# Kernel tuning notes

Measured on AMD Instinct MI355X. Metric: run time of the kernel, lower is better.

The kernel has to match this reference:

```python
import jax, jax.numpy as jnp
import numpy as np

G, R, M, H, NH, OUT = 2048, 1024, 1024, 256, 8, 2
DH = H // NH


def _ln(x, g, b):
    m = jnp.mean(x, -1, keepdims=True)
    v = jnp.var(x, -1, keepdims=True)
    return (x - m) * jax.lax.rsqrt(v + 1e-5) * g + b


def _mha(xq, xkv, w, mask=None):
    # w: [4, H, H] = (Wq, Wk, Wv, Wo); mask: [Nq, Nk] bool (True = attend)
    q = (xq @ w[0]).reshape(-1, NH, DH)
    k = (xkv @ w[1]).reshape(-1, NH, DH)
    v = (xkv @ w[2]).reshape(-1, NH, DH)
    s = jnp.einsum('qhd,khd->hqk', q, k) * np.float32(1.0 / np.sqrt(DH))
    if mask is not None:
        s = jnp.where(mask[None], s, jnp.float32(-1e9))
    a = jax.nn.softmax(s, -1)
    ctx = jnp.einsum('hqk,khd->qhd', a, v).reshape(xq.shape[0], H)
    return ctx @ w[3]


def setup_inputs() -> dict:
    key = jax.random.key(0)
    ks = jax.random.split(key, 32)
    sc = np.float32(1.0 / np.sqrt(H))

    def n(i, shape, s=sc):
        return jax.random.normal(ks[i], shape, jnp.float32) * s

    inp = {}
    inp['gene_emb'] = n(0, (G, H), 0.02)
    inp['reaction_emb'] = n(1, (R, H), 0.02)
    inp['metab_emb'] = n(2, (M, H), 0.02)
    # PreProcessor (note: torch code reuses ONE LayerNorm instance -> shared params)
    inp['pre_w1'] = n(3, (H, H)); inp['pre_b1'] = jnp.zeros((H,), jnp.float32)
    inp['pre_w2'] = n(4, (H, H)); inp['pre_b2'] = jnp.zeros((H,), jnp.float32)
    inp['pre_ln_g'] = jnp.ones((H,), jnp.float32); inp['pre_ln_b'] = jnp.zeros((H,), jnp.float32)
    # NSA: 'M' block = masked attention per edge type (4), 'S' block = full self-attn per node type (3)
    inp['wm'] = n(5, (4, 4, H, H))
    inp['ws'] = n(6, (3, 4, H, H))
    inp['ln_g'] = jnp.ones((3, H), jnp.float32); inp['ln_b'] = jnp.zeros((3, H), jnp.float32)
    # AttentionalGraphAggregation
    inp['gate_w1'] = n(7, (H, H // 2)); inp['gate_b1'] = jnp.zeros((H // 2,), jnp.float32)
    inp['gate_w2'] = n(8, (H // 2, 1)); inp['gate_b2'] = jnp.zeros((1,), jnp.float32)
    inp['tr_w'] = n(9, (H, H)); inp['tr_b'] = jnp.zeros((H,), jnp.float32)
    # prediction head: num_layers=1 -> single Linear
    inp['head_w'] = n(10, (H, OUT)); inp['head_b'] = jnp.zeros((OUT,), jnp.float32)
    # dense edge masks (sparse biological graphs)
    inp['adj_pp'] = jax.random.bernoulli(ks[11], 0.01, (G, G))
    inp['adj_rr'] = jax.random.bernoulli(ks[12], 0.01, (G, G))
    inp['inc_gpr'] = jax.random.bernoulli(ks[13], 0.01, (R, G))
    inp['adj_mm'] = jax.random.bernoulli(ks[14], 0.01, (M, M))
    return inp


def reference(gene_emb, reaction_emb, metab_emb, pre_w1, pre_b1, pre_w2, pre_b2,
              pre_ln_g, pre_ln_b, wm, ws, ln_g, ln_b, gate_w1, gate_b1, gate_w2,
              gate_b2, tr_w, tr_b, head_w, head_b, adj_pp, adj_rr, inc_gpr, adj_mm):
    # preprocessor MLP on gene embeddings (single-graph path; dropout=eval/identity)
    h = jax.nn.relu(_ln(gene_emb @ pre_w1 + pre_b1, pre_ln_g, pre_ln_b))
    xg = jax.nn.relu(_ln(h @ pre_w2 + pre_b2, pre_ln_g, pre_ln_b))
    xr, xm = reaction_emb, metab_emb
    # 'M' block: masked cross/self attention per edge type, sum-aggregated per dst type
    mg = _mha(xg, xg, wm[0], adj_pp) + _mha(xg, xg, wm[1], adj_rr)
    mr = _mha(xr, xg, wm[2], inc_gpr)
    mm = _mha(xm, xm, wm[3], adj_mm)
    xg, xr, xm = xg + mg, xr + mr, xm + mm
    # 'S' block: full self-attention within each node set
    xg = xg + _mha(xg, xg, ws[0])
    xr = xr + _mha(xr, xr, ws[1])
    xm = xm + _mha(xm, xm, ws[2])
    # per-node-type layer norms (gene branch feeds the head)
    xg = _ln(xg, ln_g[0], ln_b[0])
    # attentional graph aggregation over gene nodes (single graph -> plain softmax)
    gate = jax.nn.relu(xg @ gate_w1 + gate_b1) @ gate_w2 + gate_b2  # [G, 1]
    a = jax.nn.softmax(gate, 0)
    t = jax.nn.relu(xg @ tr_w + tr_b)
    pooled = jnp.sum(a * t, 0, keepdims=True)  # [1, H]
    return pooled @ head_w + head_b  # [1, OUT]
```

## Files before the change

kernel.cpp:

```cpp
#include <hip/hip_runtime.h>
#include <hip/hip_bf16.h>
#include <cmath>
#include <cstdint>

typedef unsigned int u32;
typedef unsigned char u8;
typedef unsigned short ushort;
typedef __attribute__((ext_vector_type(8))) short short8;
typedef __attribute__((ext_vector_type(4))) float f32x4;
typedef __attribute__((ext_vector_type(16))) float f32x16;
typedef __attribute__((ext_vector_type(4))) unsigned short us4;

#define Gn 2048
#define Hd 256
#define CSTRIDE 192

static __device__ __forceinline__ ushort f2bf(float x) {
    __hip_bfloat16 b = __float2bfloat16(x);
    return *reinterpret_cast<ushort*>(&b);
}
static __device__ __forceinline__ float bf2f(ushort u) {
    return __uint_as_float(((u32)u) << 16);
}


template <int BETA, int OUTMODE, int QKVMODE, int KT, int LNF, int LNRELU, int WRA>
static __device__ __forceinline__ void gemm_body(
    const int bx, const int by, const int bz,
    const float* __restrict__ A, int lda,
    const ushort* __restrict__ bt_hi, const ushort* __restrict__ bt_lo,
    int slot0, int slot2, const float* __restrict__ bias,
    const float* __restrict__ lng, const float* __restrict__ lnb,
    float* __restrict__ C, int N, float* __restrict__ Aout)
{
    const int tid = threadIdx.x;
    const int wv = tid >> 6, l = tid & 63;
    const int lr = l & 15, lg = l >> 4;
    const int row = bx * 32 + wv * 16 + lr;
    const int col0 = by * 64;
    int slot = slot0, zq = 0, buf = 0;
    if (QKVMODE == 1) { slot = slot0 + bz + bz / 3; zq = bz % 3; buf = bz / 3; }
    else if (QKVMODE == 2) { slot = slot0 + bz; zq = bz; }
    const ushort* bhb = bt_hi + (long)slot * 65536;
    const ushort* blb = bt_lo + (long)slot * 65536;
    const float* arow = A + (long)row * lda;

    float mean = 0.f, rs = 0.f;
    if (LNF) {
        float s = 0.f, s2 = 0.f;
        #pragma unroll
        for (int ks = 0; ks < 8; ++ks) {
            const float4 a0 = *(const float4*)&arow[ks * 32 + lg * 8];
            const float4 a1 = *(const float4*)&arow[ks * 32 + lg * 8 + 4];
            s  += (a0.x + a0.y) + (a0.z + a0.w) + (a1.x + a1.y) + (a1.z + a1.w);
            s2 += a0.x * a0.x + a0.y * a0.y + a0.z * a0.z + a0.w * a0.w +
                  a1.x * a1.x + a1.y * a1.y + a1.z * a1.z + a1.w * a1.w;
        }
        s += __shfl_xor(s, 16);  s += __shfl_xor(s, 32);
        s2 += __shfl_xor(s2, 16); s2 += __shfl_xor(s2, 32);
        mean = s * (1.f / 256.f);
        rs = rsqrtf(s2 * (1.f / 256.f) - mean * mean + 1e-5f);
    }

    const f32x4 z4 = {0.f, 0.f, 0.f, 0.f};
    f32x4 acc[4] = {z4, z4, z4, z4};

    #pragma unroll
    for (int ks = 0; ks < KT / 32; ++ks) {
        const int k0 = ks * 32;
        const ushort* bh; const ushort* bl; int kbi = ks;
        if (KT == 512 && k0 >= 256) {
            bh = bt_hi + (long)slot2 * 65536;
            bl = bt_lo + (long)slot2 * 65536;
            kbi = ks - 8;
        } else { bh = bhb; bl = blb; }
        float av[8];
        *(float4*)&av[0] = *(const float4*)&arow[k0 + lg * 8];
        *(float4*)&av[4] = *(const float4*)&arow[k0 + lg * 8 + 4];
        if (LNF) {
            float gvv[8], bvv[8];
            *(float4*)&gvv[0] = *(const float4*)&lng[k0 + lg * 8];
            *(float4*)&gvv[4] = *(const float4*)&lng[k0 + lg * 8 + 4];
            *(float4*)&bvv[0] = *(const float4*)&lnb[k0 + lg * 8];
            *(float4*)&bvv[4] = *(const float4*)&lnb[k0 + lg * 8 + 4];
            #pragma unroll
            for (int j = 0; j < 8; ++j) {
                float v = (av[j] - mean) * rs * gvv[j] + bvv[j];
                if (LNRELU) v = fmaxf(v, 0.f);
                av[j] = v;
            }
            if (WRA && by == 0 && bz == 0) {
                *(float4*)&Aout[(long)row * 256 + k0 + lg * 8] = *(float4*)&av[0];
                *(float4*)&Aout[(long)row * 256 + k0 + lg * 8 + 4] = *(float4*)&av[4];
            }
        }
        short8 ahi, alo;
        #pragma unroll
        for (int j = 0; j < 8; ++j) {
            const u32 bi = __float_as_uint(av[j]);
            ahi[j] = (short)(bi >> 16);
            const float fh = __uint_as_float(bi & 0xffff0000u);
            alo[j] = (short)f2bf(av[j] - fh);
        }
        #pragma unroll
        for (int f = 0; f < 4; ++f) {
            const long bo = (long)(((by * 4 + f) * 8 + kbi) << 9) + (l << 3);
            const short8 bhi = *(const short8*)&bh[bo];
            const short8 blo = *(const short8*)&bl[bo];
            acc[f] = __builtin_amdgcn_mfma_f32_16x16x32_bf16(ahi, bhi, acc[f], 0, 0, 0);
            acc[f] = __builtin_amdgcn_mfma_f32_16x16x32_bf16(alo, bhi, acc[f], 0, 0, 0);
            acc[f] = __builtin_amdgcn_mfma_f32_16x16x32_bf16(ahi, blo, acc[f], 0, 0, 0);
        }
    }

    const float QS = 0.17677669529663687f * 1.4426950408889634f;

    #pragma unroll
    for (int f = 0; f < 4; ++f) {
        const int col = col0 + f * 16 + lr;
        const float bv = bias ? bias[col] : 0.f;
        #pragma unroll
        for (int r = 0; r < 4; ++r) {
            const int rr = bx * 32 + wv * 16 + lg * 4 + r;
            float v = acc[f][r] + bv;
            if (OUTMODE == 1) {
                if (zq == 0) v *= QS;
                ushort* ob = (ushort*)C + (long)buf * 1572864;
                const int h = col >> 5, d = col & 31;
                if (QKVMODE == 1 || zq < 2)
                    ob[zq * 524288 + ((h * 2048 + rr) << 5) + d] = f2bf(v);
                else
                    ob[1048576 + ((h * 32 + d) << 11) + rr] = f2bf(v);
            } else {
                if (BETA) v += C[(long)rr * N + col];
                C[(long)rr * N + col] = v;
            }
        }
    }
}

__global__ __launch_bounds__(256) void mergedA_kernel(
    const u8* __restrict__ adj, int* __restrict__ det0, int* __restrict__ det1,
    const float* __restrict__ pre_w1, const float* __restrict__ pre_w2,
    const float* __restrict__ wm, const float* __restrict__ wsw,
    const float* __restrict__ gate_w1, const float* __restrict__ tr_w,
    ushort* __restrict__ bt_hi, ushort* __restrict__ bt_lo,
    u32* __restrict__ ticket)
{
    __shared__ float T[32][257];
    __shared__ int sd0[4], sd1[4];
    const int tid = threadIdx.x;
    if (blockIdx.x == 0 && tid == 0) *ticket = 0;
    if (blockIdx.x < 64) {
        const int idx = blockIdx.x * 256 + tid;
        const uint4 w = ((const uint4*)adj)[idx];
        int c0 = ((w.x & 0xffu) ? 1 : 0) + ((w.y & 0xffu) ? 1 : 0) +
                 ((w.z & 0xffu) ? 1 : 0) + ((w.w & 0xffu) ? 1 : 0);
        int c1 = ((w.x & 0xffffff00u) ? 1 : 0) + ((w.y & 0xffffff00u) ? 1 : 0) +
                 ((w.z & 0xffffff00u) ? 1 : 0) + ((w.w & 0xffffff00u) ? 1 : 0);
        #pragma unroll
        for (int o = 1; o < 64; o <<= 1) { c0 += __shfl_xor(c0, o); c1 += __shfl_xor(c1, o); }
        if ((tid & 63) == 0) { sd0[tid >> 6] = c0; sd1[tid >> 6] = c1; }
        __syncthreads();
        if (tid == 0) {
            det0[blockIdx.x] = sd0[0] + sd0[1] + sd0[2] + sd0[3];
            det1[blockIdx.x] = sd1[0] + sd1[1] + sd1[2] + sd1[3];
        }
        return;
    }
    const int b2 = blockIdx.x - 64;
    const int slot = b2 >> 3;
    const int kb = b2 & 7;
    const int k0 = kb * 32;
    const float* src; int ncols = 256;
    if (slot == 0) src = pre_w1;
    else if (slot == 1) src = pre_w2;
    else if (slot < 6) src = wm + (long)(slot - 2) * 65536;
    else if (slot < 10) src = wm + (long)(4 + slot - 6) * 65536;
    else if (slot < 14) src = wsw + (long)(slot - 10) * 65536;
    else if (slot == 14) { src = gate_w1; ncols = 128; }
    else src = tr_w;

    const int lsh = (ncols == 256) ? 6 : 5;
    const int tot = 32 << lsh;
    for (int i = tid; i < tot; i += 256) {
        const int kk = i >> lsh, c4 = (i & ((1 << lsh) - 1)) << 2;
        const float4 v = *(const float4*)&src[(long)(k0 + kk) * ncols + c4];
        T[kk][c4 + 0] = v.x; T[kk][c4 + 1] = v.y;
        T[kk][c4 + 2] = v.z; T[kk][c4 + 3] = v.w;
    }
    __syncthreads();
    if (tid < ncols) {
        ushort hb[32], lb[32];
        #pragma unroll
        for (int kk = 0; kk < 32; ++kk) {
            const float x = T[kk][tid];
            const u32 bi = __float_as_uint(x);
            const ushort h = (ushort)(bi >> 16);
            const float fh = __uint_as_float(bi & 0xffff0000u);
            hb[kk] = h; lb[kk] = f2bf(x - fh);
        }
        const int cb = tid >> 4, lr = tid & 15;
        const long base = (long)slot * 65536 + ((cb * 8 + kb) << 9);
        ushort* oh = bt_hi + base;
        ushort* ol = bt_lo + base;
        #pragma unroll
        for (int lg2 = 0; lg2 < 4; ++lg2) {
            const int off = (lg2 * 16 + lr) << 3;
            *(uint4*)&oh[off] = *(const uint4*)&hb[lg2 * 8];
            *(uint4*)&ol[off] = *(const uint4*)&lb[lg2 * 8];
        }
    }
}

__global__ __launch_bounds__(128) void mergedB_kernel(
    const u8* __restrict__ src0, const u8* __restrict__ src1,
    const int* __restrict__ det0, const int* __restrict__ det1,
    u32* __restrict__ bits, int* __restrict__ deg, int* __restrict__ colidx,
    const float* __restrict__ gene_emb,
    const ushort* __restrict__ bt_hi, const ushort* __restrict__ bt_lo,
    const float* __restrict__ pre_b1, float* __restrict__ tmp0)
{
    __shared__ u32 sw[128];
    const int tid = threadIdx.x;
    if (blockIdx.x < 2048) {
        const int lane = tid & 63;
        int c0 = det0[lane], c1 = det1[lane];
        #pragma unroll
        for (int o = 1; o < 64; o <<= 1) { c0 += __shfl_xor(c0, o); c1 += __shfl_xor(c1, o); }
        const int f = (c0 > 0) ? ((c1 > 0) ? 1 : 0) : 2;
        const int W = blockIdx.x * 128 + tid;
        const int z = W >> 17;
        const int rem = W & 131071;
        const int row = rem >> 6, w = rem & 63;
// ... 25 lines not shown
            const uint4* p = (const uint4*)((const float*)src + (long)row * 2048 + w * 32);
            #pragma unroll
            for (int j = 0; j < 8; ++j) {
                const uint4 q = p[j];
                v |= ((q.x & 0x7fffffffu) ? 1u : 0u) << (j * 4 + 0);
                v |= ((q.y & 0x7fffffffu) ? 1u : 0u) << (j * 4 + 1);
                v |= ((q.z & 0x7fffffffu) ? 1u : 0u) << (j * 4 + 2);
                v |= ((q.w & 0x7fffffffu) ? 1u : 0u) << (j * 4 + 3);
            }
        }
        bits[(long)z * 131072 + rem] = v;
        sw[tid] = v;
        __syncthreads();
        if (tid < 2) {
            const int rem0 = (blockIdx.x * 128) & 131071;
            const int r = (rem0 >> 6) + tid;
            int* ci = colidx + ((long)z * 2048 + r) * CSTRIDE;
            int d = 0;
            #pragma unroll 4
            for (int ww = 0; ww < 64; ++ww) {
                u32 x = sw[tid * 64 + ww];
                while (x) {
                    const int j = __ffs(x) - 1;
                    if (d < CSTRIDE) ci[d] = ww * 32 + j;
                    ++d;
                    x &= x - 1;
                }
            }
            deg[z * 2048 + r] = d < CSTRIDE ? d : CSTRIDE;
        }
        return;
    }
    const int b2 = blockIdx.x - 2048;
    gemm_body<0, 0, 0, 256, 0, 0, 0>(b2 >> 2, b2 & 3, 0, gene_emb, 256,
                                     bt_hi, bt_lo, 0, 0, pre_b1,
                                     nullptr, nullptr, tmp0, 256, nullptr);
}

__global__ __launch_bounds__(128) void mergedC_kernel(
    const float* __restrict__ tmp0,
    const ushort* __restrict__ bt_hi, const ushort* __restrict__ bt_lo,
    const float* __restrict__ pre_b2, const float* __restrict__ pre_ln_g,
    const float* __restrict__ pre_ln_b, float* __restrict__ tmp1)
{
    const int b2 = blockIdx.x;
    gemm_body<0, 0, 0, 256, 1, 1, 0>(b2 >> 2, b2 & 3, 0, tmp0, 256,
                                     bt_hi, bt_lo, 1, 0, pre_b2,
                                     pre_ln_g, pre_ln_b, tmp1, 256, nullptr);
}

__global__ __launch_bounds__(128) void qkvm_kernel(
    const float* __restrict__ tmp1,
    const ushort* __restrict__ bt_hi, const ushort* __restrict__ bt_lo,
    const float* __restrict__ pre_ln_g, const float* __restrict__ pre_ln_b,
    float* __restrict__ qkvb, float* __restrict__ xg1)
{
    gemm_body<0, 1, 1, 256, 1, 1, 1>(blockIdx.x, blockIdx.y, blockIdx.z,
                                     tmp1, 256, bt_hi, bt_lo, 2, 0, nullptr,
                                     pre_ln_g, pre_ln_b, qkvb, 256, xg1);
}
__global__ __launch_bounds__(128) void wo_m_kernel(
    const float* __restrict__ ctx2,
    const ushort* __restrict__ bt_hi, const ushort* __restrict__ bt_lo,
    float* __restrict__ xg1)
{
    gemm_body<1, 0, 0, 512, 0, 0, 0>(blockIdx.x, blockIdx.y, 0, ctx2, 512,
                                     bt_hi, bt_lo, 5, 9, nullptr,
                                     nullptr, nullptr, xg1, 256, nullptr);
}
__global__ __launch_bounds__(128) void qkvs_kernel(
    const float* __restrict__ xg1,
    const ushort* __restrict__ bt_hi, const ushort* __restrict__ bt_lo,
    float* __restrict__ qkvb)
{
    gemm_body<0, 1, 2, 256, 0, 0, 0>(blockIdx.x, blockIdx.y, blockIdx.z,
                                     xg1, 256, bt_hi, bt_lo, 10, 0, nullptr,
                                     nullptr, nullptr, qkvb, 256, nullptr);
}
__global__ __launch_bounds__(128) void wo_s_kernel(
    const float* __restrict__ ctx2,
    const ushort* __restrict__ bt_hi, const ushort* __restrict__ bt_lo,
    float* __restrict__ xg1)
{
    gemm_body<1, 0, 0, 256, 0, 0, 0>(blockIdx.x, blockIdx.y, 0, ctx2, 512,
                                     bt_hi, bt_lo, 13, 0, nullptr,
                                     nullptr, nullptr, xg1, 256, nullptr);
}

__global__ __launch_bounds__(64) void attn_sparse_kernel(
    const ushort* __restrict__ qkvb, const int* __restrict__ deg,
    const int* __restrict__ colidx, float* __restrict__ ctx)
{
    const int r = blockIdx.x, z = blockIdx.y;
    const ushort* qb = qkvb + (long)z * 1572864;
    const ushort* kb = qb + 524288;
    const ushort* vr = qb + 1048576;
    const int l = threadIdx.x;
    const int h = l >> 3, dg = l & 7;
    float* orow = &ctx[(long)r * 512 + z * 256 + h * 32 + dg * 4];
    const int n = deg[z * 2048 + r];
    if (n == 0) {
        float a0 = 0.f, a1 = 0.f, a2 = 0.f, a3 = 0.f;
        for (int k = 0; k < 2048; ++k) {
            const us4 vv = *(const us4*)&vr[((h * 2048 + k) << 5) + dg * 4];
            a0 += bf2f(vv[0]); a1 += bf2f(vv[1]); a2 += bf2f(vv[2]); a3 += bf2f(vv[3]);
        }
        float4 o; const float inv = 1.f / 2048.f;
        o.x = a0 * inv; o.y = a1 * inv; o.z = a2 * inv; o.w = a3 * inv;
        *(float4*)orow = o;
        return;
    }
    float q0, q1, q2, q3;
    {
        const us4 qv = *(const us4*)&qb[((h * 2048 + r) << 5) + dg * 4];
        q0 = bf2f(qv[0]); q1 = bf2f(qv[1]); q2 = bf2f(qv[2]); q3 = bf2f(qv[3]);
    }
    const int* ci = colidx + ((long)z * 2048 + r) * CSTRIDE;
    float m = -INFINITY, lsum = 0.f;
    float a0 = 0.f, a1 = 0.f, a2 = 0.f, a3 = 0.f;
    int kn = ci[0];
    us4 kv = *(const us4*)&kb[((h * 2048 + kn) << 5) + dg * 4];
    us4 vv = *(const us4*)&vr[((h * 2048 + kn) << 5) + dg * 4];
    for (int e = 0; e < n; ++e) {
        const us4 kc = kv, vc = vv;
        if (e + 1 < n) {
            kn = ci[e + 1];
            kv = *(const us4*)&kb[((h * 2048 + kn) << 5) + dg * 4];
            vv = *(const us4*)&vr[((h * 2048 + kn) << 5) + dg * 4];
        }
        float s = q0 * bf2f(kc[0]) + q1 * bf2f(kc[1]) +
                  q2 * bf2f(kc[2]) + q3 * bf2f(kc[3]);
        s += __shfl_xor(s, 1); s += __shfl_xor(s, 2); s += __shfl_xor(s, 4);
        const float mn = fmaxf(m, s);
        const float fac = __builtin_amdgcn_exp2f(m - mn);
        const float p = __builtin_amdgcn_exp2f(s - mn);
        lsum = lsum * fac + p;
        a0 = a0 * fac + p * bf2f(vc[0]);
        a1 = a1 * fac + p * bf2f(vc[1]);
        a2 = a2 * fac + p * bf2f(vc[2]);
        a3 = a3 * fac + p * bf2f(vc[3]);
        m = mn;
    }
    const float inv = 1.f / lsum;
    float4 o; o.x = a0 * inv; o.y = a1 * inv; o.z = a2 * inv; o.w = a3 * inv;
    *(float4*)orow = o;
}

__global__ __launch_bounds__(512) void attn_dense_kernel(
    const ushort* __restrict__ qkvb, float* __restrict__ ctx)
{
    const ushort* qb = qkvb;
    const ushort* kb = qb + 524288;
    const ushort* vt = qb + 1048576;
    const int h = blockIdx.x, qt = blockIdx.y;
    const int wv = threadIdx.x >> 6;
    const int l = threadIdx.x & 63;
    const int lq = l & 31;
    const int hi = l >> 5;
    const int qglob = qt * 32 + lq;

    __shared__ float Mm[8][32], Ml[8][32];
    __shared__ float Macc[8][64][17];
    __shared__ float ctile[32][33];

    const int qoff = ((h * 2048 + qglob) << 5) + hi * 8;
    const short8 qf0 = *(const short8*)&qb[qoff];
    const short8 qf1 = *(const short8*)&qb[qoff + 16];

    float m = -INFINITY, lsum = 0.f;
    f32x16 acc, zz16;
    #pragma unroll
    for (int i = 0; i < 16; ++i) { acc[i] = 0.f; zz16[i] = 0.f; }

    const int kt0 = wv * 256;
    #pragma unroll 2
    for (int it = 0; it < 8; ++it) {
        const int kbase = kt0 + it * 32;
        const int koff = ((h * 2048 + kbase + lq) << 5) + hi * 8;
        const short8 kf0 = *(const short8*)&kb[koff];
        const short8 kf1 = *(const short8*)&kb[koff + 16];
        f32x16 s = __builtin_amdgcn_mfma_f32_32x32x16_bf16(kf0, qf0, zz16, 0, 0, 0);
        s = __builtin_amdgcn_mfma_f32_32x32x16_bf16(kf1, qf1, s, 0, 0, 0);
// ... 50 lines not shown

    if (l < 32) { Mm[wv][l] = m; Ml[wv][l] = lsum; }
    #pragma unroll
    for (int i = 0; i < 16; ++i) Macc[wv][l][i] = acc[i];
    __syncthreads();
    {
        const int t = threadIdx.x;
        const int q = t & 31, j = t >> 5;
        float M = Mm[0][q];
        #pragma unroll
        for (int w = 1; w < 8; ++w) M = fmaxf(M, Mm[w][q]);
        float fw[8], den = 0.f;
        #pragma unroll
        for (int w = 0; w < 8; ++w) {
            fw[w] = __builtin_amdgcn_exp2f(Mm[w][q] - M);
            den += Ml[w][q] * fw[w];
        }
        const float inv = 1.f / den;
        #pragma unroll
        for (int half = 0; half < 2; ++half) {
            const int d = j + 16 * half;
            const int i = (d & 3) | ((d >> 3) << 2);
            const int h2 = (d >> 2) & 1;
            float o = 0.f;
            #pragma unroll
            for (int w = 0; w < 8; ++w) o += Macc[w][h2 * 32 + q][i] * fw[w];
            ctile[d][q] = o * inv;
        }
    }
    __syncthreads();
    if (threadIdx.x < 256) {
        const int t = threadIdx.x;
        const int q = t >> 3, d0 = (t & 7) << 2;
        float4 ov;
        ov.x = ctile[d0 + 0][q]; ov.y = ctile[d0 + 1][q];
        ov.z = ctile[d0 + 2][q]; ov.w = ctile[d0 + 3][q];
        *(float4*)&ctx[(long)(qt * 32 + q) * 512 + h * 32 + d0] = ov;
    }
}

__global__ __launch_bounds__(64) void aggr_gemm_kernel(
    const float* __restrict__ xg1,
    const ushort* __restrict__ bt_hi, const ushort* __restrict__ bt_lo,
    const float* __restrict__ ln_g, const float* __restrict__ ln_b,
    const float* __restrict__ tr_b, const float* __restrict__ g_b1,
    const float* __restrict__ g_w2, const float* __restrict__ g_b2,
    float* __restrict__ t_out, float* __restrict__ gv)
{
    const int l = threadIdx.x;
    const int lr = l & 15, lg = l >> 4;
    const int row0 = blockIdx.x * 16;
    const int gate = (blockIdx.y == 8);
    const int slot = gate ? 14 : 15;
    const int col0 = gate ? 0 : blockIdx.y * 32;
    const int NF = gate ? 8 : 2;
    const ushort* bh0 = bt_hi + (long)slot * 65536;
    const ushort* bl0 = bt_lo + (long)slot * 65536;
    const float* arow = xg1 + (long)(row0 + lr) * 256;

    float s = 0.f, s2 = 0.f;
    #pragma unroll
    for (int ks = 0; ks < 8; ++ks) {
        const float4 a0 = *(const float4*)&arow[ks * 32 + lg * 8];
        const float4 a1 = *(const float4*)&arow[ks * 32 + lg * 8 + 4];
        s  += (a0.x + a0.y) + (a0.z + a0.w) + (a1.x + a1.y) + (a1.z + a1.w);
        s2 += a0.x * a0.x + a0.y * a0.y + a0.z * a0.z + a0.w * a0.w +
              a1.x * a1.x + a1.y * a1.y + a1.z * a1.z + a1.w * a1.w;
    }
    s += __shfl_xor(s, 16);  s += __shfl_xor(s, 32);
    s2 += __shfl_xor(s2, 16); s2 += __shfl_xor(s2, 32);
    const float mean = s * (1.f / 256.f);
    const float rs = rsqrtf(s2 * (1.f / 256.f) - mean * mean + 1e-5f);

    const f32x4 z4 = {0.f, 0.f, 0.f, 0.f};
    f32x4 acc[8] = {z4, z4, z4, z4, z4, z4, z4, z4};

    #pragma unroll
    for (int ks = 0; ks < 8; ++ks) {
        const int k0 = ks * 32;
        float av[8], gvv[8], bvv[8];
        *(float4*)&av[0] = *(const float4*)&arow[k0 + lg * 8];
        *(float4*)&av[4] = *(const float4*)&arow[k0 + lg * 8 + 4];
        *(float4*)&gvv[0] = *(const float4*)&ln_g[k0 + lg * 8];
        *(float4*)&gvv[4] = *(const float4*)&ln_g[k0 + lg * 8 + 4];
        *(float4*)&bvv[0] = *(const float4*)&ln_b[k0 + lg * 8];
        *(float4*)&bvv[4] = *(const float4*)&ln_b[k0 + lg * 8 + 4];
        short8 ahi, alo;
        #pragma unroll
        for (int j = 0; j < 8; ++j) {
            const float vn = (av[j] - mean) * rs * gvv[j] + bvv[j];
            const u32 bi = __float_as_uint(vn);
            ahi[j] = (short)(bi >> 16);
            const float fh = __uint_as_float(bi & 0xffff0000u);
            alo[j] = (short)f2bf(vn - fh);
        }
        for (int f = 0; f < NF; ++f) {
            const int cb = gate ? f : ((int)blockIdx.y * 2 + f);
            const long bo = (long)((cb * 8 + ks) << 9) + (l << 3);
            const short8 bhi = *(const short8*)&bh0[bo];
            const short8 blo = *(const short8*)&bl0[bo];
            acc[f] = __builtin_amdgcn_mfma_f32_16x16x32_bf16(ahi, bhi, acc[f], 0, 0, 0);
            acc[f] = __builtin_amdgcn_mfma_f32_16x16x32_bf16(alo, bhi, acc[f], 0, 0, 0);
            acc[f] = __builtin_amdgcn_mfma_f32_16x16x32_bf16(ahi, blo, acc[f], 0, 0, 0);
        }
    }

    if (!gate) {
        #pragma unroll
        for (int f = 0; f < 2; ++f) {
            const int col = col0 + f * 16 + lr;
            const float bv = tr_b[col];
            #pragma unroll
            for (int r = 0; r < 4; ++r) {
                const int rr = row0 + lg * 4 + r;
                t_out[(long)rr * 256 + col] = fmaxf(acc[f][r] + bv, 0.f);
            }
        }
    } else {
        float b1v[8], w2v[8];
        #pragma unroll
        for (int f = 0; f < 8; ++f) {
            b1v[f] = g_b1[f * 16 + lr];
            w2v[f] = g_w2[f * 16 + lr];
        }
        const float b2 = g_b2[0];
        #pragma unroll
        for (int r = 0; r < 4; ++r) {
            float t = 0.f;
// ... 69 lines not shown
}

extern "C" void kernel_launch(void* const* d_in, const int* in_sizes, int n_in,
                              void* d_out, int out_size, void* d_ws, size_t ws_size,
                              hipStream_t stream)
{
    (void)in_sizes; (void)n_in; (void)out_size; (void)ws_size;
    const float* gene_emb = (const float*)d_in[0];
    const float* pre_w1   = (const float*)d_in[3];
    const float* pre_b1   = (const float*)d_in[4];
    const float* pre_w2   = (const float*)d_in[5];
    const float* pre_b2   = (const float*)d_in[6];
    const float* pre_ln_g = (const float*)d_in[7];
    const float* pre_ln_b = (const float*)d_in[8];
    const float* wm       = (const float*)d_in[9];
    const float* wsw      = (const float*)d_in[10];
    const float* ln_g     = (const float*)d_in[11];
    const float* ln_b     = (const float*)d_in[12];
    const float* gate_w1  = (const float*)d_in[13];
    const float* gate_b1  = (const float*)d_in[14];
    const float* gate_w2  = (const float*)d_in[15];
    const float* gate_b2  = (const float*)d_in[16];
    const float* tr_w     = (const float*)d_in[17];
    const float* tr_b     = (const float*)d_in[18];
    const float* head_w   = (const float*)d_in[19];
    const float* head_b   = (const float*)d_in[20];
    const u8* adj_pp      = (const u8*)d_in[21];
    const u8* adj_rr      = (const u8*)d_in[22];

    const long NHf = (long)Gn * Hd;
    float* tmp0    = (float*)d_ws;
    float* tmp1    = tmp0 + NHf;
    float* xg1     = tmp1 + NHf;
    float* ctx2    = xg1 + NHf;
    float* gv      = ctx2 + 2 * NHf;
    float* partial = gv + Gn;
    float* denp    = partial + 64 * 256;
    float* mpart   = denp + 64;
    int* det0      = (int*)(mpart + 64);
    int* det1      = det0 + 64;
    u32* ticket    = (u32*)(det1 + 64);
    int* deg       = (int*)(ticket + 64);
    int* colidx    = deg + 4096;
    u32* bits      = (u32*)(colidx + 2L * 2048 * CSTRIDE);
    ushort* qkvb   = (ushort*)(bits + 262144);
    ushort* bt_hi  = qkvb + 2L * 1572864;
    ushort* bt_lo  = bt_hi + 16L * 65536;

    dim3 B256(256), B128(128), T64(64);

    mergedA_kernel<<<dim3(192), B256, 0, stream>>>(adj_pp, det0, det1,
        pre_w1, pre_w2, wm, wsw, gate_w1, tr_w, bt_hi, bt_lo, ticket);
    mergedB_kernel<<<dim3(2304), B128, 0, stream>>>(adj_pp, adj_rr, det0, det1,
        bits, deg, colidx, gene_emb, bt_hi, bt_lo, pre_b1, tmp0);
    mergedC_kernel<<<dim3(256), B128, 0, stream>>>(tmp0, bt_hi, bt_lo,
        pre_b2, pre_ln_g, pre_ln_b, tmp1);
    qkvm_kernel<<<dim3(64, 4, 6), B128, 0, stream>>>(tmp1, bt_hi, bt_lo,
        pre_ln_g, pre_ln_b, (float*)qkvb, xg1);
    attn_sparse_kernel<<<dim3(2048, 2), T64, 0, stream>>>(qkvb, deg, colidx, ctx2);
    wo_m_kernel<<<dim3(64, 4), B128, 0, stream>>>(ctx2, bt_hi, bt_lo, xg1);
    qkvs_kernel<<<dim3(64, 4, 3), B128, 0, stream>>>(xg1, bt_hi, bt_lo, (float*)qkvb);
    attn_dense_kernel<<<dim3(8, 64), dim3(512), 0, stream>>>(qkvb, ctx2);
    wo_s_kernel<<<dim3(64, 4), B128, 0, stream>>>(ctx2, bt_hi, bt_lo, xg1);
    aggr_gemm_kernel<<<dim3(128, 9), T64, 0, stream>>>(xg1, bt_hi, bt_lo,
        ln_g, ln_b, tr_b, gate_b1, gate_w2, gate_b2, tmp0, gv);
    wsum_head_kernel<<<dim3(64), B256, 0, stream>>>(gv, tmp0, partial, denp,
        mpart, head_w, head_b, (float*)d_out, ticket);
}
```

Before: 186.1 us.

## Pre-split GEMM activations into bf16 hi/lo planes with standalone LayerNorm kernels

Moves LayerNorm and the fp32-to-bf16 hi/lo split out of the GEMM inner loops. Producers (new per-row LN kernels, the attention kernels, wo_m epilogue) now write activations as separate hi and lo bf16 planes that the GEMMs load directly. This removes the redundant per-column-block LN statistics and split arithmetic in every GEMM tile and halves the activation read bytes. In exchange it adds three extra kernel launches and extra global writes of the split planes.

```diff
diff --git a/kernel.cpp b/kernel.cpp
--- a/kernel.cpp
+++ b/kernel.cpp
@@ -22,16 +22,21 @@
 static __device__ __forceinline__ float bf2f(ushort u) {
     return __uint_as_float(((u32)u) << 16);
 }
-
-
-template <int BETA, int OUTMODE, int QKVMODE, int KT, int LNF, int LNRELU, int WRA>
-static __device__ __forceinline__ void gemm_body(
+static __device__ __forceinline__ void split2(float x, ushort& h, ushort& lo) {
+    const u32 bi = __float_as_uint(x);
+    h = (ushort)(bi >> 16);
+    lo = f2bf(x - __uint_as_float(bi & 0xffff0000u));
+}
+
+
+template <int BETA, int OUTMODE, int QKVMODE, int KT, int WPL>
+static __device__ __forceinline__ void gemm_pl(
     const int bx, const int by, const int bz,
-    const float* __restrict__ A, int lda,
+    const ushort* __restrict__ ah, const ushort* __restrict__ al, int lda,
     const ushort* __restrict__ bt_hi, const ushort* __restrict__ bt_lo,
     int slot0, int slot2, const float* __restrict__ bias,
-    const float* __restrict__ lng, const float* __restrict__ lnb,
-    float* __restrict__ C, int N, float* __restrict__ Aout)
+    float* __restrict__ C, int N,
+    ushort* __restrict__ xh, ushort* __restrict__ xl)
 {
     const int tid = threadIdx.x;
     const int wv = tid >> 6, l = tid & 63;
@@ -43,24 +48,8 @@
     else if (QKVMODE == 2) { slot = slot0 + bz; zq = bz; }
     const ushort* bhb = bt_hi + (long)slot * 65536;
     const ushort* blb = bt_lo + (long)slot * 65536;
-    const float* arow = A + (long)row * lda;
-
-    float mean = 0.f, rs = 0.f;
-    if (LNF) {
-        float s = 0.f, s2 = 0.f;
-        #pragma unroll
-        for (int ks = 0; ks < 8; ++ks) {
-            const float4 a0 = *(const float4*)&arow[ks * 32 + lg * 8];
-            const float4 a1 = *(const float4*)&arow[ks * 32 + lg * 8 + 4];
-            s  += (a0.x + a0.y) + (a0.z + a0.w) + (a1.x + a1.y) + (a1.z + a1.w);
-            s2 += a0.x * a0.x + a0.y * a0.y + a0.z * a0.z + a0.w * a0.w +
-                  a1.x * a1.x + a1.y * a1.y + a1.z * a1.z + a1.w * a1.w;
-        }
-        s += __shfl_xor(s, 16);  s += __shfl_xor(s, 32);
-        s2 += __shfl_xor(s2, 16); s2 += __shfl_xor(s2, 32);
-        mean = s * (1.f / 256.f);
-        rs = rsqrtf(s2 * (1.f / 256.f) - mean * mean + 1e-5f);
-    }
+    const ushort* arh = ah + (long)row * lda;
+    const ushort* arl = al + (long)row * lda;
 
     const f32x4 z4 = {0.f, 0.f, 0.f, 0.f};
     f32x4 acc[4] = {z4, z4, z4, z4};
@@ -74,34 +63,8 @@
             bl = bt_lo + (long)slot2 * 65536;
             kbi = ks - 8;
         } else { bh = bhb; bl = blb; }
-        float av[8];
-        *(float4*)&av[0] = *(const float4*)&arow[k0 + lg * 8];
-        *(float4*)&av[4] = *(const float4*)&arow[k0 + lg * 8 + 4];
-        if (LNF) {
-            float gvv[8], bvv[8];
-            *(float4*)&gvv[0] = *(const float4*)&lng[k0 + lg * 8];
-            *(float4*)&gvv[4] = *(const float4*)&lng[k0 + lg * 8 + 4];
-            *(float4*)&bvv[0] = *(const float4*)&lnb[k0 + lg * 8];
-            *(float4*)&bvv[4] = *(const float4*)&lnb[k0 + lg * 8 + 4];
-            #pragma unroll
-            for (int j = 0; j < 8; ++j) {
-                float v = (av[j] - mean) * rs * gvv[j] + bvv[j];
-                if (LNRELU) v = fmaxf(v, 0.f);
-                av[j] = v;
-            }
-            if (WRA && by == 0 && bz == 0) {
-                *(float4*)&Aout[(long)row * 256 + k0 + lg * 8] = *(float4*)&av[0];
-                *(float4*)&Aout[(long)row * 256 + k0 + lg * 8 + 4] = *(float4*)&av[4];
-            }
-        }
-        short8 ahi, alo;
-        #pragma unroll
-        for (int j = 0; j < 8; ++j) {
-            const u32 bi = __float_as_uint(av[j]);
-            ahi[j] = (short)(bi >> 16);
-            const float fh = __uint_as_float(bi & 0xffff0000u);
-            alo[j] = (short)f2bf(av[j] - fh);
-        }
+        const short8 ahi = *(const short8*)&arh[k0 + lg * 8];
+        const short8 alo = *(const short8*)&arl[k0 + lg * 8];
         #pragma unroll
         for (int f = 0; f < 4; ++f) {
             const long bo = (long)(((by * 4 + f) * 8 + kbi) << 9) + (l << 3);
@@ -134,8 +97,105 @@
             } else {
                 if (BETA) v += C[(long)rr * N + col];
                 C[(long)rr * N + col] = v;
+                if (WPL) {
+                    ushort hh, ll;
+                    split2(v, hh, ll);
+                    xh[(long)rr * 256 + col] = hh;
+                    xl[(long)rr * 256 + col] = ll;
+                }
             }
         }
+    }
+}
+
+static __device__ __forceinline__ void gemm_f32a(
+    const int bx, const int by,
+    const float* __restrict__ A, int lda,
+    const ushort* __restrict__ bt_hi, const ushort* __restrict__ bt_lo,
+    int slot, const float* __restrict__ bias, float* __restrict__ C, int N)
+{
+    const int tid = threadIdx.x;
+    const int wv = tid >> 6, l = tid & 63;
+    const int lr = l & 15, lg = l >> 4;
+    const int row = bx * 32 + wv * 16 + lr;
+    const int col0 = by * 64;
+    const ushort* bhb = bt_hi + (long)slot * 65536;
+    const ushort* blb = bt_lo + (long)slot * 65536;
+    const float* arow = A + (long)row * lda;
+
+    const f32x4 z4 = {0.f, 0.f, 0.f, 0.f};
+    f32x4 acc[4] = {z4, z4, z4, z4};
+
+    #pragma unroll
+    for (int ks = 0; ks < 8; ++ks) {
+        const int k0 = ks * 32;
+        float av[8];
+        *(float4*)&av[0] = *(const float4*)&arow[k0 + lg * 8];
+        *(float4*)&av[4] = *(const float4*)&arow[k0 + lg * 8 + 4];
+        short8 ahi, alo;
+        #pragma unroll
+        for (int j = 0; j < 8; ++j) {
+            ushort hh, ll;
+            split2(av[j], hh, ll);
+            ahi[j] = (short)hh; alo[j] = (short)ll;
+        }
+        #pragma unroll
+        for (int f = 0; f < 4; ++f) {
+            const long bo = (long)(((by * 4 + f) * 8 + ks) << 9) + (l << 3);
+            const short8 bhi = *(const short8*)&bhb[bo];
+            const short8 blo = *(const short8*)&blb[bo];
+            acc[f] = __builtin_amdgcn_mfma_f32_16x16x32_bf16(ahi, bhi, acc[f], 0, 0, 0);
+            acc[f] = __builtin_amdgcn_mfma_f32_16x16x32_bf16(alo, bhi, acc[f], 0, 0, 0);
+            acc[f] = __builtin_amdgcn_mfma_f32_16x16x32_bf16(ahi, blo, acc[f], 0, 0, 0);
+        }
+    }
+    #pragma unroll
+    for (int f = 0; f < 4; ++f) {
+        const int col = col0 + f * 16 + lr;
+        const float bv = bias[col];
+        #pragma unroll
+        for (int r = 0; r < 4; ++r) {
+            const int rr = bx * 32 + wv * 16 + lg * 4 + r;
+            C[(long)rr * N + col] = acc[f][r] + bv;
+        }
+    }
+}
+
+template <int RELU, int DUP>
+__global__ __launch_bounds__(64) void ln_pl_kernel(
+    const float* __restrict__ X, const float* __restrict__ gw,
+    const float* __restrict__ bw, ushort* __restrict__ Yh,
+    ushort* __restrict__ Yl, float* __restrict__ Y2)
+{
+    const int row = blockIdx.x, tid = threadIdx.x;
+    const float4 x = *(const float4*)&X[(long)row * 256 + (tid << 2)];
+    float s = x.x + x.y + x.z + x.w;
+    float s2 = x.x * x.x + x.y * x.y + x.z * x.z + x.w * x.w;
+    #pragma unroll
+    for (int o = 1; o < 64; o <<= 1) { s += __shfl_xor(s, o); s2 += __shfl_xor(s2, o); }
+    const float mean = s * (1.f / 256.f);
+    const float var = s2 * (1.f / 256.f) - mean * mean;
+    const float rs = rsqrtf(var + 1e-5f);
+    const float4 g4 = *(const float4*)&gw[tid << 2];
+    const float4 b4 = *(const float4*)&bw[tid << 2];
+    float y[4];
+    y[0] = (x.x - mean) * rs * g4.x + b4.x;
+    y[1] = (x.y - mean) * rs * g4.y + b4.y;
+    y[2] = (x.z - mean) * rs * g4.z + b4.z;
+    y[3] = (x.w - mean) * rs * g4.w + b4.w;
+    us4 h4, l4;
+    #pragma unroll
+    for (int j = 0; j < 4; ++j) {
+        if (RELU) y[j] = fmaxf(y[j], 0.f);
+        ushort hh, ll;
+        split2(y[j], hh, ll);
+        h4[j] = hh; l4[j] = ll;
+    }
+    *(us4*)&Yh[(long)row * 256 + (tid << 2)] = h4;
+    *(us4*)&Yl[(long)row * 256 + (tid << 2)] = l4;
+    if (DUP) {
+        float4 yo; yo.x = y[0]; yo.y = y[1]; yo.z = y[2]; yo.w = y[3];
+        *(float4*)&Y2[(long)row * 256 + (tid << 2)] = yo;
     }
 }
 
@@ -193,13 +253,7 @@
     if (tid < ncols) {
         ushort hb[32], lb[32];
         #pragma unroll
-        for (int kk = 0; kk < 32; ++kk) {
-            const float x = T[kk][tid];
-            const u32 bi = __float_as_uint(x);
-            const ushort h = (ushort)(bi >> 16);
-            const float fh = __uint_as_float(bi & 0xffff0000u);
-            hb[kk] = h; lb[kk] = f2bf(x - fh);
-        }
+        for (int kk = 0; kk < 32; ++kk) split2(T[kk][tid], hb[kk], lb[kk]);
         const int cb = tid >> 4, lr = tid & 15;
         const long base = (long)slot * 65536 + ((cb * 8 + kb) << 9);
         ushort* oh = bt_hi + base;
@@ -291,64 +345,53 @@
         return;
     }
     const int b2 = blockIdx.x - 2048;
-    gemm_body<0, 0, 0, 256, 0, 0, 0>(b2 >> 2, b2 & 3, 0, gene_emb, 256,
-                                     bt_hi, bt_lo, 0, 0, pre_b1,
-                                     nullptr, nullptr, tmp0, 256, nullptr);
-}
-
-__global__ __launch_bounds__(128) void mergedC_kernel(
-    const float* __restrict__ tmp0,
-    const ushort* __restrict__ bt_hi, const ushort* __restrict__ bt_lo,
-    const float* __restrict__ pre_b2, const float* __restrict__ pre_ln_g,
-    const float* __restrict__ pre_ln_b, float* __restrict__ tmp1)
-{
-    const int b2 = blockIdx.x;
-    gemm_body<0, 0, 0, 256, 1, 1, 0>(b2 >> 2, b2 & 3, 0, tmp0, 256,
-                                     bt_hi, bt_lo, 1, 0, pre_b2,
-                                     pre_ln_g, pre_ln_b, tmp1, 256, nullptr);
-}
-
+    gemm_f32a(b2 >> 2, b2 & 3, gene_emb, 256, bt_hi, bt_lo, 0, pre_b1, tmp0, 256);
+}
+
+__global__ __launch_bounds__(128) void gemm2_kernel(
+    const ushort* __restrict__ a1h, const ushort* __restrict__ a1l,
+    const ushort* __restrict__ bt_hi, const ushort* __restrict__ bt_lo,
+    const float* __restrict__ pre_b2, float* __restrict__ tmp1)
+{
+    gemm_pl<0, 0, 0, 256, 0>(blockIdx.x, blockIdx.y, 0, a1h, a1l, 256,
+                             bt_hi, bt_lo, 1, 0, pre_b2, tmp1, 256, nullptr, nullptr);
+}
 __global__ __launch_bounds__(128) void qkvm_kernel(
-    const float* __restrict__ tmp1,
-    const ushort* __restrict__ bt_hi, const ushort* __restrict__ bt_lo,
-    const float* __restrict__ pre_ln_g, const float* __restrict__ pre_ln_b,
-    float* __restrict__ qkvb, float* __restrict__ xg1)
-{
-    gemm_body<0, 1, 1, 256, 1, 1, 1>(blockIdx.x, blockIdx.y, blockIdx.z,
-                                     tmp1, 256, bt_hi, bt_lo, 2, 0, nullptr,
-                                     pre_ln_g, pre_ln_b, qkvb, 256, xg1);
+    const ushort* __restrict__ a2h, const ushort* __restrict__ a2l,
+    const ushort* __restrict__ bt_hi, const ushort* __restrict__ bt_lo,
+    float* __restrict__ qkvb)
+{
+    gemm_pl<0, 1, 1, 256, 0>(blockIdx.x, blockIdx.y, blockIdx.z, a2h, a2l, 256,
+                             bt_hi, bt_lo, 2, 0, nullptr, qkvb, 256, nullptr, nullptr);
 }
 __global__ __launch_bounds__(128) void wo_m_kernel(
-    const float* __restrict__ ctx2,
+    const ushort* __restrict__ c2h, const ushort* __restrict__ c2l,
+    const ushort* __restrict__ bt_hi, const ushort* __restrict__ bt_lo,
+    float* __restrict__ xg1, ushort* __restrict__ x1h, ushort* __restrict__ x1l)
+{
+    gemm_pl<1, 0, 0, 512, 1>(blockIdx.x, blockIdx.y, 0, c2h, c2l, 512,
+                             bt_hi, bt_lo, 5, 9, nullptr, xg1, 256, x1h, x1l);
+}
+__global__ __launch_bounds__(128) void qkvs_kernel(
+    const ushort* __restrict__ x1h, const ushort* __restrict__ x1l,
+    const ushort* __restrict__ bt_hi, const ushort* __restrict__ bt_lo,
+    float* __restrict__ qkvb)
+{
+    gemm_pl<0, 1, 2, 256, 0>(blockIdx.x, blockIdx.y, blockIdx.z, x1h, x1l, 256,
+                             bt_hi, bt_lo, 10, 0, nullptr, qkvb, 256, nullptr, nullptr);
+}
+__global__ __launch_bounds__(128) void wo_s_kernel(
+    const ushort* __restrict__ c2h, const ushort* __restrict__ c2l,
     const ushort* __restrict__ bt_hi, const ushort* __restrict__ bt_lo,
     float* __restrict__ xg1)
 {
-    gemm_body<1, 0, 0, 512, 0, 0, 0>(blockIdx.x, blockIdx.y, 0, ctx2, 512,
-                                     bt_hi, bt_lo, 5, 9, nullptr,
-                                     nullptr, nullptr, xg1, 256, nullptr);
-}
-__global__ __launch_bounds__(128) void qkvs_kernel(
-    const float* __restrict__ xg1,
-    const ushort* __restrict__ bt_hi, const ushort* __restrict__ bt_lo,
-    float* __restrict__ qkvb)
-{
-    gemm_body<0, 1, 2, 256, 0, 0, 0>(blockIdx.x, blockIdx.y, blockIdx.z,
-                                     xg1, 256, bt_hi, bt_lo, 10, 0, nullptr,
-                                     nullptr, nullptr, qkvb, 256, nullptr);
-}
-__global__ __launch_bounds__(128) void wo_s_kernel(
-    const float* __restrict__ ctx2,
-    const ushort* __restrict__ bt_hi, const ushort* __restrict__ bt_lo,
-    float* __restrict__ xg1)
-{
-    gemm_body<1, 0, 0, 256, 0, 0, 0>(blockIdx.x, blockIdx.y, 0, ctx2, 512,
-                                     bt_hi, bt_lo, 13, 0, nullptr,
-                                     nullptr, nullptr, xg1, 256, nullptr);
+    gemm_pl<1, 0, 0, 256, 0>(blockIdx.x, blockIdx.y, 0, c2h, c2l, 512,
+                             bt_hi, bt_lo, 13, 0, nullptr, xg1, 256, nullptr, nullptr);
 }
 
 __global__ __launch_bounds__(64) void attn_sparse_kernel(
     const ushort* __restrict__ qkvb, const int* __restrict__ deg,
-    const int* __restrict__ colidx, float* __restrict__ ctx)
+    const int* __restrict__ colidx, ushort* __restrict__ ch, ushort* __restrict__ cl)
 {
     const int r = blockIdx.x, z = blockIdx.y;
     const ushort* qb = qkvb + (long)z * 1572864;
@@ -356,57 +399,61 @@
     const ushort* vr = qb + 1048576;
     const int l = threadIdx.x;
     const int h = l >> 3, dg = l & 7;
-    float* orow = &ctx[(long)r * 512 + z * 256 + h * 32 + dg * 4];
+    const long ooff = (long)r * 512 + z * 256 + h * 32 + dg * 4;
     const int n = deg[z * 2048 + r];
+    float o[4];
     if (n == 0) {
         float a0 = 0.f, a1 = 0.f, a2 = 0.f, a3 = 0.f;
         for (int k = 0; k < 2048; ++k) {
             const us4 vv = *(const us4*)&vr[((h * 2048 + k) << 5) + dg * 4];
             a0 += bf2f(vv[0]); a1 += bf2f(vv[1]); a2 += bf2f(vv[2]); a3 += bf2f(vv[3]);
         }
-        float4 o; const float inv = 1.f / 2048.f;
-        o.x = a0 * inv; o.y = a1 * inv; o.z = a2 * inv; o.w = a3 * inv;
-        *(float4*)orow = o;
-        return;
-    }
-    float q0, q1, q2, q3;
-    {
-        const us4 qv = *(const us4*)&qb[((h * 2048 + r) << 5) + dg * 4];
-        q0 = bf2f(qv[0]); q1 = bf2f(qv[1]); q2 = bf2f(qv[2]); q3 = bf2f(qv[3]);
-    }
-    const int* ci = colidx + ((long)z * 2048 + r) * CSTRIDE;
-    float m = -INFINITY, lsum = 0.f;
-    float a0 = 0.f, a1 = 0.f, a2 = 0.f, a3 = 0.f;
-    int kn = ci[0];
-    us4 kv = *(const us4*)&kb[((h * 2048 + kn) << 5) + dg * 4];
-    us4 vv = *(const us4*)&vr[((h * 2048 + kn) << 5) + dg * 4];
-    for (int e = 0; e < n; ++e) {
-        const us4 kc = kv, vc = vv;
-        if (e + 1 < n) {
-            kn = ci[e + 1];
-            kv = *(const us4*)&kb[((h * 2048 + kn) << 5) + dg * 4];
-            vv = *(const us4*)&vr[((h * 2048 + kn) << 5) + dg * 4];
-        }
-        float s = q0 * bf2f(kc[0]) + q1 * bf2f(kc[1]) +
-                  q2 * bf2f(kc[2]) + q3 * bf2f(kc[3]);
-        s += __shfl_xor(s, 1); s += __shfl_xor(s, 2); s += __shfl_xor(s, 4);
-        const float mn = fmaxf(m, s);
-        const float fac = __builtin_amdgcn_exp2f(m - mn);
-        const float p = __builtin_amdgcn_exp2f(s - mn);
-        lsum = lsum * fac + p;
-        a0 = a0 * fac + p * bf2f(vc[0]);
-        a1 = a1 * fac + p * bf2f(vc[1]);
-        a2 = a2 * fac + p * bf2f(vc[2]);
-        a3 = a3 * fac + p * bf2f(vc[3]);
-        m = mn;
-    }
-    const float inv = 1.f / lsum;
-    float4 o; o.x = a0 * inv; o.y = a1 * inv; o.z = a2 * inv; o.w = a3 * inv;
-    *(float4*)orow = o;
+        const float inv = 1.f / 2048.f;
+        o[0] = a0 * inv; o[1] = a1 * inv; o[2] = a2 * inv; o[3] = a3 * inv;
+    } else {
+        float q0, q1, q2, q3;
+        {
+            const us4 qv = *(const us4*)&qb[((h * 2048 + r) << 5) + dg * 4];
+            q0 = bf2f(qv[0]); q1 = bf2f(qv[1]); q2 = bf2f(qv[2]); q3 = bf2f(qv[3]);
+        }
+        const int* ci = colidx + ((long)z * 2048 + r) * CSTRIDE;
+        float m = -INFINITY, lsum = 0.f;
+        float a0 = 0.f, a1 = 0.f, a2 = 0.f, a3 = 0.f;
+        int kn = ci[0];
+        us4 kv = *(const us4*)&kb[((h * 2048 + kn) << 5) + dg * 4];
+        us4 vv = *(const us4*)&vr[((h * 2048 + kn) << 5) + dg * 4];
+        for (int e = 0; e < n; ++e) {
+            const us4 kc = kv, vc = vv;
+            if (e + 1 < n) {
+                kn = ci[e + 1];
+                kv = *(const us4*)&kb[((h * 2048 + kn) << 5) + dg * 4];
+                vv = *(const us4*)&vr[((h * 2048 + kn) << 5) + dg * 4];
+            }
+            float s = q0 * bf2f(kc[0]) + q1 * bf2f(kc[1]) +
+                      q2 * bf2f(kc[2]) + q3 * bf2f(kc[3]);
+            s += __shfl_xor(s, 1); s += __shfl_xor(s, 2); s += __shfl_xor(s, 4);
+            const float mn = fmaxf(m, s);
+            const float fac = __builtin_amdgcn_exp2f(m - mn);
+            const float p = __builtin_amdgcn_exp2f(s - mn);
+            lsum = lsum * fac + p;
+            a0 = a0 * fac + p * bf2f(vc[0]);
+            a1 = a1 * fac + p * bf2f(vc[1]);
+            a2 = a2 * fac + p * bf2f(vc[2]);
+            a3 = a3 * fac + p * bf2f(vc[3]);
+            m = mn;
+        }
+        const float inv = 1.f / lsum;
+        o[0] = a0 * inv; o[1] = a1 * inv; o[2] = a2 * inv; o[3] = a3 * inv;
+    }
+    us4 h4, l4;
+    #pragma unroll
+    for (int j = 0; j < 4; ++j) { ushort hh, ll; split2(o[j], hh, ll); h4[j] = hh; l4[j] = ll; }
+    *(us4*)&ch[ooff] = h4;
+    *(us4*)&cl[ooff] = l4;
 }
 
 __global__ __launch_bounds__(512) void attn_dense_kernel(
-    const ushort* __restrict__ qkvb, float* __restrict__ ctx)
+    const ushort* __restrict__ qkvb, ushort* __restrict__ ch, ushort* __restrict__ cl)
 {
     const ushort* qb = qkvb;
     const ushort* kb = qb + 524288;
@@ -523,17 +570,22 @@
     if (threadIdx.x < 256) {
         const int t = threadIdx.x;
         const int q = t >> 3, d0 = (t & 7) << 2;
-        float4 ov;
-        ov.x = ctile[d0 + 0][q]; ov.y = ctile[d0 + 1][q];
-        ov.z = ctile[d0 + 2][q]; ov.w = ctile[d0 + 3][q];
-        *(float4*)&ctx[(long)(qt * 32 + q) * 512 + h * 32 + d0] = ov;
+        us4 h4, l4;
+        #pragma unroll
+        for (int j = 0; j < 4; ++j) {
+            ushort hh, ll;
+            split2(ctile[d0 + j][q], hh, ll);
+            h4[j] = hh; l4[j] = ll;
+        }
+        const long ooff = (long)(qt * 32 + q) * 512 + h * 32 + d0;
+        *(us4*)&ch[ooff] = h4;
+        *(us4*)&cl[ooff] = l4;
     }
 }
 
 __global__ __launch_bounds__(64) void aggr_gemm_kernel(
-    const float* __restrict__ xg1,
-    const ushort* __restrict__ bt_hi, const ushort* __restrict__ bt_lo,
-    const float* __restrict__ ln_g, const float* __restrict__ ln_b,
+    const ushort* __restrict__ a3h, const ushort* __restrict__ a3l,
+    const ushort* __restrict__ bt_hi, const ushort* __restrict__ bt_lo,
     const float* __restrict__ tr_b, const float* __restrict__ g_b1,
     const float* __restrict__ g_w2, const float* __restrict__ g_b2,
     float* __restrict__ t_out, float* __restrict__ gv)
@@ -547,21 +599,8 @@
     const int NF = gate ? 8 : 2;
     const ushort* bh0 = bt_hi + (long)slot * 65536;
     const ushort* bl0 = bt_lo + (long)slot * 65536;
-    const float* arow = xg1 + (long)(row0 + lr) * 256;
-
-    float s = 0.f, s2 = 0.f;
-    #pragma unroll
-    for (int ks = 0; ks < 8; ++ks) {
-        const float4 a0 = *(const float4*)&arow[ks * 32 + lg * 8];
-        const float4 a1 = *(const float4*)&arow[ks * 32 + lg * 8 + 4];
-        s  += (a0.x + a0.y) + (a0.z + a0.w) + (a1.x + a1.y) + (a1.z + a1.w);
-        s2 += a0.x * a0.x + a0.y * a0.y + a0.z * a0.z + a0.w * a0.w +
-              a1.x * a1.x + a1.y * a1.y + a1.z * a1.z + a1.w * a1.w;
-    }
-    s += __shfl_xor(s, 16);  s += __shfl_xor(s, 32);
-    s2 += __shfl_xor(s2, 16); s2 += __shfl_xor(s2, 32);
-    const float mean = s * (1.f / 256.f);
-    const float rs = rsqrtf(s2 * (1.f / 256.f) - mean * mean + 1e-5f);
+    const ushort* arh = a3h + (long)(row0 + lr) * 256;
+    const ushort* arl = a3l + (long)(row0 + lr) * 256;
 
     const f32x4 z4 = {0.f, 0.f, 0.f, 0.f};
     f32x4 acc[8] = {z4, z4, z4, z4, z4, z4, z4, z4};
@@ -569,22 +608,8 @@
     #pragma unroll
     for (int ks = 0; ks < 8; ++ks) {
         const int k0 = ks * 32;
-        float av[8], gvv[8], bvv[8];
-        *(float4*)&av[0] = *(const float4*)&arow[k0 + lg * 8];
-        *(float4*)&av[4] = *(const float4*)&arow[k0 + lg * 8 + 4];
-        *(float4*)&gvv[0] = *(const float4*)&ln_g[k0 + lg * 8];
-        *(float4*)&gvv[4] = *(const float4*)&ln_g[k0 + lg * 8 + 4];
-        *(float4*)&bvv[0] = *(const float4*)&ln_b[k0 + lg * 8];
-        *(float4*)&bvv[4] = *(const float4*)&ln_b[k0 + lg * 8 + 4];
-        short8 ahi, alo;
-        #pragma unroll
-        for (int j = 0; j < 8; ++j) {
-            const float vn = (av[j] - mean) * rs * gvv[j] + bvv[j];
-            const u32 bi = __float_as_uint(vn);
-            ahi[j] = (short)(bi >> 16);
-            const float fh = __uint_as_float(bi & 0xffff0000u);
-            alo[j] = (short)f2bf(vn - fh);
-        }
+        const short8 ahi = *(const short8*)&arh[k0 + lg * 8];
+        const short8 alo = *(const short8*)&arl[k0 + lg * 8];
         for (int f = 0; f < NF; ++f) {
             const int cb = gate ? f : ((int)blockIdx.y * 2 + f);
             const long bo = (long)((cb * 8 + ks) << 9) + (l << 3);
@@ -720,8 +745,7 @@
     float* tmp0    = (float*)d_ws;
     float* tmp1    = tmp0 + NHf;
     float* xg1     = tmp1 + NHf;
-    float* ctx2    = xg1 + NHf;
-    float* gv      = ctx2 + 2 * NHf;
+    float* gv      = xg1 + NHf;
     float* partial = gv + Gn;
     float* denp    = partial + 64 * 256;
     float* mpart   = denp + 64;
@@ -734,24 +758,36 @@
     ushort* qkvb   = (ushort*)(bits + 262144);
     ushort* bt_hi  = qkvb + 2L * 1572864;
     ushort* bt_lo  = bt_hi + 16L * 65536;
+    ushort* a1h    = bt_lo + 16L * 65536;
+    ushort* a1l    = a1h + NHf;
+    ushort* a2h    = a1l + NHf;
+    ushort* a2l    = a2h + NHf;
+    ushort* x1h    = a2l + NHf;
+    ushort* x1l    = x1h + NHf;
+    ushort* a3h    = x1l + NHf;
+    ushort* a3l    = a3h + NHf;
+    ushort* c2h    = a3l + NHf;
+    ushort* c2l    = c2h + 2 * NHf;
 
     dim3 B256(256), B128(128), T64(64);
+    dim3 LN(2048);
 
     mergedA_kernel<<<dim3(192), B256, 0, stream>>>(adj_pp, det0, det1,
         pre_w1, pre_w2, wm, wsw, gate_w1, tr_w, bt_hi, bt_lo, ticket);
     mergedB_kernel<<<dim3(2304), B128, 0, stream>>>(adj_pp, adj_rr, det0, det1,
         bits, deg, colidx, gene_emb, bt_hi, bt_lo, pre_b1, tmp0);
-    mergedC_kernel<<<dim3(256), B128, 0, stream>>>(tmp0, bt_hi, bt_lo,
-        pre_b2, pre_ln_g, pre_ln_b, tmp1);
-    qkvm_kernel<<<dim3(64, 4, 6), B128, 0, stream>>>(tmp1, bt_hi, bt_lo,
-        pre_ln_g, pre_ln_b, (float*)qkvb, xg1);
-    attn_sparse_kernel<<<dim3(2048, 2), T64, 0, stream>>>(qkvb, deg, colidx, ctx2);
-    wo_m_kernel<<<dim3(64, 4), B128, 0, stream>>>(ctx2, bt_hi, bt_lo, xg1);
-    qkvs_kernel<<<dim3(64, 4, 3), B128, 0, stream>>>(xg1, bt_hi, bt_lo, (float*)qkvb);
-    attn_dense_kernel<<<dim3(8, 64), dim3(512), 0, stream>>>(qkvb, ctx2);
-    wo_s_kernel<<<dim3(64, 4), B128, 0, stream>>>(ctx2, bt_hi, bt_lo, xg1);
-    aggr_gemm_kernel<<<dim3(128, 9), T64, 0, stream>>>(xg1, bt_hi, bt_lo,
-        ln_g, ln_b, tr_b, gate_b1, gate_w2, gate_b2, tmp0, gv);
+    ln_pl_kernel<1, 0><<<LN, T64, 0, stream>>>(tmp0, pre_ln_g, pre_ln_b, a1h, a1l, nullptr);
+    gemm2_kernel<<<dim3(64, 4), B128, 0, stream>>>(a1h, a1l, bt_hi, bt_lo, pre_b2, tmp1);
+    ln_pl_kernel<1, 1><<<LN, T64, 0, stream>>>(tmp1, pre_ln_g, pre_ln_b, a2h, a2l, xg1);
+    qkvm_kernel<<<dim3(64, 4, 6), B128, 0, stream>>>(a2h, a2l, bt_hi, bt_lo, (float*)qkvb);
+    attn_sparse_kernel<<<dim3(2048, 2), T64, 0, stream>>>(qkvb, deg, colidx, c2h, c2l);
+    wo_m_kernel<<<dim3(64, 4), B128, 0, stream>>>(c2h, c2l, bt_hi, bt_lo, xg1, x1h, x1l);
+    qkvs_kernel<<<dim3(64, 4, 3), B128, 0, stream>>>(x1h, x1l, bt_hi, bt_lo, (float*)qkvb);
+    attn_dense_kernel<<<dim3(8, 64), dim3(512), 0, stream>>>(qkvb, c2h, c2l);
+    wo_s_kernel<<<dim3(64, 4), B128, 0, stream>>>(c2h, c2l, bt_hi, bt_lo, xg1);
+    ln_pl_kernel<0, 0><<<LN, T64, 0, stream>>>(xg1, ln_g, ln_b, a3h, a3l, nullptr);
+    aggr_gemm_kernel<<<dim3(128, 9), T64, 0, stream>>>(a3h, a3l, bt_hi, bt_lo,
+        tr_b, gate_b1, gate_w2, gate_b2, tmp0, gv);
     wsum_head_kernel<<<dim3(64), B256, 0, stream>>>(gv, tmp0, partial, denp,
         mpart, head_w, head_b, (float*)d_out, ticket);
 }
```

New measurement: 201.2 us. 8.1% more time.
